# Optimization experiments

Hardware: AMD Instinct MI355X
Metric: run time of the kernel (lower is better)

Reference implementation:

```python
import jax, jax.numpy as jnp
import numpy as np

WORD_DICT_SIZE = 50002
POS_DICT_SIZE = 53
DEP_DICT_SIZE = 54
EMB = 128
UNITS = 100
B, T = 256, 256
IN_DIM = 3 * EMB  # 384


def setup_inputs() -> dict:
    key = jax.random.key(0)
    ks = jax.random.split(key, 12)
    words = jax.random.randint(ks[0], (B, T), 1, WORD_DICT_SIZE)
    pos = jax.random.randint(ks[1], (B, T), 1, POS_DICT_SIZE)
    dep = jax.random.randint(ks[2], (B, T), 1, DEP_DICT_SIZE)
    # ragged padding: index 0 is the mask token (mask_zero=True)
    lengths = jax.random.randint(ks[3], (B,), T // 2, T + 1)
    pad = jnp.arange(T)[None, :] >= lengths[:, None]
    words = jnp.where(pad, 0, words)
    pos = jnp.where(pad, 0, pos)
    dep = jnp.where(pad, 0, dep)

    def glorot(k, shape):
        lim = np.sqrt(6.0 / (shape[0] + shape[1]))
        return jax.random.uniform(k, shape, jnp.float32, -lim, lim)

    E_word = glorot(ks[4], (WORD_DICT_SIZE, EMB))
    E_pos = glorot(ks[5], (POS_DICT_SIZE, EMB))
    E_dep = glorot(ks[6], (DEP_DICT_SIZE, EMB))
    W_fwd = glorot(ks[7], (IN_DIM, 4 * UNITS))
    U_fwd = glorot(ks[8], (UNITS, 4 * UNITS))
    W_bwd = glorot(ks[9], (IN_DIM, 4 * UNITS))
    U_bwd = glorot(ks[10], (UNITS, 4 * UNITS))
    # Keras unit_forget_bias=True: forget-gate bias initialized to 1
    b = jnp.zeros((4 * UNITS,), jnp.float32).at[UNITS:2 * UNITS].set(1.0)
    W_out = glorot(ks[11], (2 * UNITS, 1))
    b_out = jnp.zeros((1,), jnp.float32)
    return {"words": words, "pos": pos, "dep": dep,
            "E_word": E_word, "E_pos": E_pos, "E_dep": E_dep,
            "W_fwd": W_fwd, "U_fwd": U_fwd, "b_fwd": b,
            "W_bwd": W_bwd, "U_bwd": U_bwd, "b_bwd": b,
            "W_out": W_out, "b_out": b_out}


def _masked_lstm(x_tbd, mask_tb, W, U, b, reverse):
    """Keras-style masked LSTM. x_tbd: [T,B,D], mask_tb: [T,B].
    Masked steps carry state/output through unchanged (zero_output_for_mask=False)."""
    units = U.shape[0]
    xw = jnp.einsum('tbd,dh->tbh', x_tbd, W) + b  # precompute input projection

    def step(carry, inp):
        h, c = carry
        xw_t, m = inp
        z = xw_t + h @ U
        i, f, g, o = jnp.split(z, 4, axis=-1)
        i = jax.nn.sigmoid(i)
        f = jax.nn.sigmoid(f)
        g = jnp.tanh(g)
        o = jax.nn.sigmoid(o)
        c_new = f * c + i * g
        h_new = o * jnp.tanh(c_new)
        m = m[:, None]
        h2 = jnp.where(m, h_new, h)
        c2 = jnp.where(m, c_new, c)
        return (h2, c2), h2

    h0 = jnp.zeros((x_tbd.shape[1], units), x_tbd.dtype)
    _, hs = jax.lax.scan(step, (h0, h0), (xw, mask_tb), reverse=reverse)
    return hs  # [T,B,units]


def reference(words, pos, dep, E_word, E_pos, E_dep,
              W_fwd, U_fwd, b_fwd, W_bwd, U_bwd, b_bwd, W_out, b_out):
    mask = words != 0  # [B,T]
    x = jnp.concatenate([E_word[words], E_pos[pos], E_dep[dep]], axis=-1)  # [B,T,384]
    xt = jnp.transpose(x, (1, 0, 2))  # [T,B,384]
    mt = mask.T                        # [T,B]
    h_f = _masked_lstm(xt, mt, W_fwd, U_fwd, b_fwd, reverse=False)
    h_b = _masked_lstm(xt, mt, W_bwd, U_bwd, b_bwd, reverse=True)
    h = jnp.concatenate([h_f, h_b], axis=-1)          # [T,B,200]
    h = jnp.transpose(h, (1, 0, 2))                    # [B,T,200]
    out = jax.nn.sigmoid(h @ W_out + b_out)[..., 0]    # [B,T]
    return out
```

## Files before the change

### kernel.cpp

```cpp
#include <hip/hip_runtime.h>
#include <hip/hip_bf16.h>

#define T_LEN 256
#define B_SZ  256
#define EMB   128
#define UNITS 100
#define GATES 400
#define NCOL  800
#define NQ    52

typedef __attribute__((ext_vector_type(8))) short short8v;
typedef __attribute__((ext_vector_type(4))) short short4v;
typedef __attribute__((ext_vector_type(4))) float f32x4;
typedef _Float16 half2v __attribute__((ext_vector_type(2)));

static __device__ __forceinline__ float bf2f(short s) {
    unsigned u = ((unsigned)(unsigned short)s) << 16;
    return __builtin_bit_cast(float, u);
}
static __device__ __forceinline__ short f2bf(float f) {
    return __builtin_bit_cast(short, __float2bfloat16(f));
}
static __device__ __forceinline__ float fast_sigmoid(float x) {
    return 1.f / (1.f + __expf(-x));
}
static __device__ __forceinline__ float fast_tanh(float x) {
    return 1.f - 2.f / (1.f + __expf(2.f * x));
}
static __device__ __forceinline__ float fdot2p(unsigned hp, unsigned up, float c) {
#if __has_builtin(__builtin_amdgcn_fdot2)
    return __builtin_amdgcn_fdot2(__builtin_bit_cast(half2v, hp),
                                  __builtin_bit_cast(half2v, up), c, false);
#else
    const half2v a = __builtin_bit_cast(half2v, hp);
    const half2v b = __builtin_bit_cast(half2v, up);
    return fmaf((float)a[1], (float)b[1], fmaf((float)a[0], (float)b[0], c));
#endif
}

#define PREP_WT_BLOCKS 100
#define PREP_TAB_BLOCKS 107
#define PREP_UPK_BLOCKS 21

__global__ __launch_bounds__(256) void prep(
    const float* __restrict__ Wf, const float* __restrict__ Wb,
    const float* __restrict__ bf_, const float* __restrict__ bb_,
    const float* __restrict__ Ep, const float* __restrict__ Ed,
    const float* __restrict__ Uf, const float* __restrict__ Ub,
    __hip_bfloat16* __restrict__ WbT, float* __restrict__ Ppos,
    float* __restrict__ Pdep, unsigned* __restrict__ Upk, int* __restrict__ flag)
{
    __shared__ short Ap[16 * 32];
    __shared__ short Bp[32 * 16];

    const int bx = blockIdx.x, tid = threadIdx.x;

    if (bx < PREP_WT_BLOCKS) {
        const int base = bx * 1024 + tid * 4;
#pragma unroll
        for (int q = 0; q < 4; ++q) {
            const int id = base + q;
            const int c = id >> 7, k = id & 127;
            const int dir = c >= GATES;
            const int j = c - dir * GATES;
            const float* W = dir ? Wb : Wf;
            WbT[id] = __float2bfloat16(W[k * GATES + j]);
        }
    } else if (bx < PREP_WT_BLOCKS + PREP_TAB_BLOCKS) {
        const int p = bx - PREP_WT_BLOCKS;
        const bool isPos = p < 53;
        const float* Erow = isPos ? (Ep + p * EMB) : (Ed + (size_t)(p - 53) * EMB);
        const int rowoff = isPos ? EMB : 2 * EMB;
        float* dst = isPos ? (Ppos + (size_t)p * NCOL) : (Pdep + (size_t)(p - 53) * NCOL);
        for (int c = tid; c < NCOL; c += 256) {
            const int dir = c >= GATES;
            const int j = c - dir * GATES;
            const float* W = dir ? Wb : Wf;
            float s = 0.f;
            for (int k = 0; k < EMB; ++k)
                s = fmaf(Erow[k], W[(size_t)(rowoff + k) * GATES + j], s);
            if (!isPos) s += (dir ? bb_[j] : bf_[j]);
            dst[c] = s;
        }
    } else if (bx < PREP_WT_BLOCKS + PREP_TAB_BLOCKS + PREP_UPK_BLOCKS) {
        const int p2 = bx - PREP_WT_BLOCKS - PREP_TAB_BLOCKS;
#pragma unroll
        for (int i = 0; i < 8; ++i) {
            const int e = p2 * 2048 + tid * 8 + i;
            if (e < 2 * NQ * GATES) {
                const int dir = e / (NQ * GATES);
                const int rem = e - dir * (NQ * GATES);
                const int q = rem / GATES, col = rem - q * GATES;
                const float* U = dir ? Ub : Uf;
                const int k0 = 2 * q, k1 = 2 * q + 1;
                const float v0 = (k0 < UNITS) ? U[(size_t)k0 * GATES + col] : 0.f;
                const float v1 = (k1 < UNITS) ? U[(size_t)k1 * GATES + col] : 0.f;
                const unsigned lo = (unsigned)(unsigned short)__builtin_bit_cast(short, (_Float16)v0);
                const unsigned hi = (unsigned)(unsigned short)__builtin_bit_cast(short, (_Float16)v1);
                Upk[e] = lo | (hi << 16);
            }
        }
    } else {
        if (tid < 64) {
            for (int e = tid; e < 512; e += 64) {
                const int m = e >> 5, k = e & 31;
                Ap[e] = f2bf((float)((m * 3 + k * 5) % 7 - 3));
            }
            for (int e = tid; e < 512; e += 64) {
                const int k = e >> 4, n = e & 15;
                Bp[e] = f2bf((float)((k * 7 + n * 3) % 5 - 2));
            }
        }
        __syncthreads();
        if (tid < 64) {
            const int l = tid, mn = l & 15, grp = l >> 4;
            float ref[4];
#pragma unroll
            for (int i = 0; i < 4; ++i) {
                const int m = grp * 4 + i;
                float s = 0.f;
                for (int k = 0; k < 32; ++k)
                    s += bf2f(Ap[m * 32 + k]) * bf2f(Bp[k * 16 + mn]);
                ref[i] = s;
            }
            short8v a8, b8;
#pragma unroll
            for (int e = 0; e < 8; ++e) {
                const int k8 = grp * 8 + e;
                a8[e] = Ap[mn * 32 + k8];
                b8[e] = Bp[k8 * 16 + mn];
            }
            f32x4 z = {0.f, 0.f, 0.f, 0.f};
            f32x4 d8 = __builtin_amdgcn_mfma_f32_16x16x32_bf16(a8, b8, z, 0, 0, 0);
            const bool ok8 = (d8[0] == ref[0]) && (d8[1] == ref[1]) &&
                             (d8[2] == ref[2]) && (d8[3] == ref[3]);
            const unsigned long long m8 = __ballot(ok8);
            if (tid == 0) flag[0] = (m8 == ~0ULL) ? 0 : 1;
        }
    }
}

#define MT 64
#define NT 160

__global__ __launch_bounds__(256) void embed_gemm(
    const int* __restrict__ words, const int* __restrict__ pos, const int* __restrict__ dep,
    const float* __restrict__ Ew, const __hip_bfloat16* __restrict__ WbT,
    const float* __restrict__ Ppos, const float* __restrict__ Pdep,
    const int* __restrict__ flag, __hip_bfloat16* __restrict__ xw)
{
    __shared__ __align__(16) short As[MT * 128];
    __shared__ __align__(16) short Bs[NT * 128];
    __shared__ int widx[MT], pidx[MT], didx[MT];

    const int tid = threadIdx.x;
    const int bx = blockIdx.x, by = blockIdx.y;
    const int r0 = bx * MT;
    const int t = r0 >> 8, b0 = r0 & 255;
    const int n0 = by * NT;

    if (tid < MT)             widx[tid]          = words[(size_t)(b0 + tid) * T_LEN + t];
    else if (tid < 2 * MT)    pidx[tid - MT]     = pos[(size_t)(b0 + tid - MT) * T_LEN + t];
    else if (tid < 3 * MT)    didx[tid - 2 * MT] = dep[(size_t)(b0 + tid - 2 * MT) * T_LEN + t];
    __syncthreads();

#pragma unroll
    for (int q = 0; q < 4; ++q) {
        const int ch = tid + q * 256;
        const int row = ch >> 4, c16 = ch & 15;
        const float* src = Ew + (size_t)widx[row] * EMB + c16 * 8;
        const float4 v0 = *reinterpret_cast<const float4*>(src);
        const float4 v1 = *reinterpret_cast<const float4*>(src + 4);
        short8v pk;
        pk[0] = f2bf(v0.x); pk[1] = f2bf(v0.y); pk[2] = f2bf(v0.z); pk[3] = f2bf(v0.w);
        pk[4] = f2bf(v1.x); pk[5] = f2bf(v1.y); pk[6] = f2bf(v1.z); pk[7] = f2bf(v1.w);
        *reinterpret_cast<short8v*>(&As[row * 128 + ((c16 ^ (row & 7)) << 3)]) = pk;
    }
#pragma unroll
    for (int q = 0; q < 10; ++q) {
        const int ch = tid + q * 256;
        const int col = ch >> 4, c16 = ch & 15;
        const short* src = reinterpret_cast<const short*>(WbT) + (size_t)(n0 + col) * 128 + c16 * 8;
        const short8v v = *reinterpret_cast<const short8v*>(src);
        *reinterpret_cast<short8v*>(&Bs[col * 128 + ((c16 ^ (col & 7)) << 3)]) = v;
    }
    __syncthreads();

    const int w = tid >> 6, l = tid & 63;
    const int lr = l & 15, lg = l >> 4;
    const int arow = w * 16 + lr;

    f32x4 acc[10];
#pragma unroll
    for (int ni = 0; ni < 10; ++ni) acc[ni] = f32x4{0.f, 0.f, 0.f, 0.f};

    const int lay = flag[0];

    if (lay == 0) {
#pragma unroll
        for (int kk = 0; kk < 4; ++kk) {
            const int c16 = kk * 4 + lg;
            const short8v a = *reinterpret_cast<const short8v*>(
                &As[arow * 128 + ((c16 ^ (arow & 7)) << 3)]);
#pragma unroll
            for (int ni = 0; ni < 10; ++ni) {
                const int col = ni * 16 + lr;
                const short8v bfr = *reinterpret_cast<const short8v*>(
                    &Bs[col * 128 + ((c16 ^ (col & 7)) << 3)]);
                acc[ni] = __builtin_amdgcn_mfma_f32_16x16x32_bf16(a, bfr, acc[ni], 0, 0, 0);
            }
        }
    } else {
#pragma unroll
        for (int kk = 0; kk < 4; ++kk) {
            const int ch16 = kk * 4 + (lg >> 1);
            const int inner = (lg & 1) * 4;
            const int alo_i = arow * 128 + ((ch16 ^ (arow & 7)) << 3) + inner;
            const int ahi_i = arow * 128 + (((ch16 + 2) ^ (arow & 7)) << 3) + inner;
            const short4v alo = *reinterpret_cast<const short4v*>(&As[alo_i]);
            const short4v ahi = *reinterpret_cast<const short4v*>(&As[ahi_i]);
            short8v a;
            a[0] = alo[0]; a[1] = alo[1]; a[2] = alo[2]; a[3] = alo[3];
            a[4] = ahi[0]; a[5] = ahi[1]; a[6] = ahi[2]; a[7] = ahi[3];
#pragma unroll
            for (int ni = 0; ni < 10; ++ni) {
                const int col = ni * 16 + lr;
                const int blo_i = col * 128 + ((ch16 ^ (col & 7)) << 3) + inner;
                const int bhi_i = col * 128 + (((ch16 + 2) ^ (col & 7)) << 3) + inner;
                const short4v blo = *reinterpret_cast<const short4v*>(&Bs[blo_i]);
                const short4v bhi = *reinterpret_cast<const short4v*>(&Bs[bhi_i]);
                short8v b;
                b[0] = blo[0]; b[1] = blo[1]; b[2] = blo[2]; b[3] = blo[3];
                b[4] = bhi[0]; b[5] = bhi[1]; b[6] = bhi[2]; b[7] = bhi[3];
                acc[ni] = __builtin_amdgcn_mfma_f32_16x16x32_bf16(a, b, acc[ni], 0, 0, 0);
            }
        }
    }

    const int rbase = w * 16 + lg * 4;
    int pix[4], dix[4];
#pragma unroll
    for (int i = 0; i < 4; ++i) { pix[i] = pidx[rbase + i]; dix[i] = didx[rbase + i]; }
#pragma unroll
    for (int ni = 0; ni < 10; ++ni) {
        const int c = n0 + ni * 16 + lr;
#pragma unroll
        for (int i = 0; i < 4; ++i) {
            const float v = acc[ni][i]
                          + Ppos[(size_t)pix[i] * NCOL + c]
                          + Pdep[(size_t)dix[i] * NCOL + c];
            xw[(size_t)(r0 + rbase + i) * NCOL + c] = __float2bfloat16(v);
        }
    }
}

#define BAR() do { \
    asm volatile("s_waitcnt lgkmcnt(0)" ::: "memory"); \
    __builtin_amdgcn_sched_barrier(0); \
    __builtin_amdgcn_s_barrier(); \
    __builtin_amdgcn_sched_barrier(0); \
} while (0)

__global__ __launch_bounds__(512, 1) void lstm_valu(
    const int* __restrict__ words,
    const __hip_bfloat16* __restrict__ xw,
    const unsigned* __restrict__ Upk,
    _Float16* __restrict__ h_f, _Float16* __restrict__ h_b)
{
    const int b = blockIdx.x >> 1, dirv = blockIdx.x & 1;
    _Float16* hout = dirv ? h_b : h_f;
    const int coff = dirv * GATES;
    const unsigned* up = Upk + (size_t)dirv * NQ * GATES;

    __shared__ __align__(16) _Float16 h_sh[104];
    __shared__ float z_sh[GATES];
    __shared__ unsigned char m_sh[T_LEN];
    __shared__ int len_sh;

    const int tid = threadIdx.x;
    const bool isCol = tid < GATES;
    const int colid = isCol ? tid : (GATES - 1);

    for (int i = tid; i < T_LEN; i += 512)
        m_sh[i] = (unsigned char)(words[(size_t)b * T_LEN + i] != 0);
    if (tid < 52) reinterpret_cast<unsigned*>(h_sh)[tid] = 0u;

    unsigned upk[NQ];
#pragma unroll
    for (int q = 0; q < NQ; ++q) upk[q] = up[q * GATES + colid];
#pragma unroll
    for (int q = 0; q < NQ; ++q) asm volatile("" : "+v"(upk[q]));

    float c = 0.f, h = 0.f;
    __syncthreads();

    if (tid == 0) {
        int fmi = T_LEN;
        for (int t = 0; t < T_LEN; ++t) if (!m_sh[t]) { fmi = t; break; }
        int ok = 1;
        for (int t = fmi; t < T_LEN; ++t) if (m_sh[t]) { ok = 0; break; }
        len_sh = ok ? fmi : T_LEN;
    }
    __syncthreads();
    const int len = len_sh;

    const short* xs = reinterpret_cast<const short*>(xw);

    if (dirv && tid < UNITS) {
        for (int t = len; t < T_LEN; ++t)
            hout[((size_t)t * B_SZ + b) * UNITS + tid] = (_Float16)0.f;
    }

    short pf = 0;
    if (isCol && len > 0) {
        const int tfirst = dirv ? (len - 1) : 0;
        pf = xs[((size_t)tfirst * B_SZ + b) * NCOL + coff + tid];
    }

    for (int s = 0; s < len; ++s) {
        const int t = dirv ? (len - 1 - s) : s;
        int tn = dirv ? (t - 1) : (t + 1);
        tn = tn < 0 ? 0 : (tn > T_LEN - 1 ? T_LEN - 1 : tn);

        short pfn = pf;
        if (isCol) {
            const float zx = bf2f(pf);
            pfn = xs[((size_t)tn * B_SZ + b) * NCOL + coff + tid];
            float a0 = 0.f, a1 = 0.f, a2 = 0.f, a3 = 0.f;
            const uint4* h4 = reinterpret_cast<const uint4*>(h_sh);
#pragma unroll
            for (int qq = 0; qq < 13; ++qq) {
                const uint4 hv = h4[qq];
                a0 = fdot2p(hv.x, upk[4 * qq + 0], a0);
                a1 = fdot2p(hv.y, upk[4 * qq + 1], a1);
                a2 = fdot2p(hv.z, upk[4 * qq + 2], a2);
                a3 = fdot2p(hv.w, upk[4 * qq + 3], a3);
            }
            z_sh[tid] = zx + (a0 + a1) + (a2 + a3);
        }
        pf = pfn;

        BAR();

        if (tid < UNITS) {
            const float zi = z_sh[tid];
            const float zf = z_sh[tid + UNITS];
            const float zg = z_sh[tid + 2 * UNITS];
            const float zo = z_sh[tid + 3 * UNITS];
            const float ig = fast_sigmoid(zi);
            const float fg = fast_sigmoid(zf);
            const float gg = fast_tanh(zg);
            const float og = fast_sigmoid(zo);
            const float cn = fg * c + ig * gg;
            const float hn = og * fast_tanh(cn);
            const bool  m  = m_sh[t] != 0;
            h = m ? hn : h;
            c = m ? cn : c;
            const _Float16 hh = (_Float16)h;
            h_sh[tid] = hh;
            hout[((size_t)t * B_SZ + b) * UNITS + tid] = hh;
        }

        BAR();
    }

    if (!dirv && tid < UNITS) {
        const _Float16 hh = (_Float16)h;
        for (int t = len; t < T_LEN; ++t)
            hout[((size_t)t * B_SZ + b) * UNITS + tid] = hh;
    }
}

__global__ __launch_bounds__(256) void out_proj(
    const _Float16* __restrict__ h_f, const _Float16* __restrict__ h_b,
    const float* __restrict__ Wo, const float* __restrict__ bo,
    float* __restrict__ out)
{
    const int tid = threadIdx.x;
    const int g = tid >> 2, sub = tid & 3;
    const int r = blockIdx.x * 64 + g;
    const int t = r >> 8, b = r & 255;

    const _Float16* hf = h_f + (size_t)r * UNITS;
    const _Float16* hb = h_b + (size_t)r * UNITS;

    float s = 0.f;
    const int k0 = sub * 25;
#pragma unroll
    for (int k = 0; k < 25; ++k) s = fmaf((float)hf[k0 + k], Wo[k0 + k], s);
#pragma unroll
    for (int k = 0; k < 25; ++k) s = fmaf((float)hb[k0 + k], Wo[UNITS + k0 + k], s);

    s += __shfl_xor(s, 1);
    s += __shfl_xor(s, 2);

    if (sub == 0)
        out[(size_t)b * T_LEN + t] = 1.f / (1.f + __expf(-(s + bo[0])));
}

extern "C" void kernel_launch(void* const* d_in, const int* in_sizes, int n_in,
                              void* d_out, int out_size, void* d_ws, size_t ws_size,
                              hipStream_t stream)
{
    const int*   words = (const int*)d_in[0];
    const int*   pos   = (const int*)d_in[1];
    const int*   dep   = (const int*)d_in[2];
    const float* Ew    = (const float*)d_in[3];
    const float* Ep    = (const float*)d_in[4];
    const float* Ed    = (const float*)d_in[5];
    const float* Wf    = (const float*)d_in[6];
    const float* Uf    = (const float*)d_in[7];
    const float* bf_   = (const float*)d_in[8];
    const float* Wb    = (const float*)d_in[9];
    const float* Ub    = (const float*)d_in[10];
    const float* bb_   = (const float*)d_in[11];
    const float* Wo    = (const float*)d_in[12];
    const float* bo    = (const float*)d_in[13];
    float* out = (float*)d_out;

    auto alignup = [](size_t x) { return (x + 255) & ~(size_t)255; };
    char* p = (char*)d_ws;
    __hip_bfloat16* xw = (__hip_bfloat16*)p;  p += alignup((size_t)T_LEN * B_SZ * NCOL * 2);
    _Float16* h_f = (_Float16*)p;             p += alignup((size_t)T_LEN * B_SZ * UNITS * 2);
    _Float16* h_b = (_Float16*)p;             p += alignup((size_t)T_LEN * B_SZ * UNITS * 2);
    __hip_bfloat16* WbT = (__hip_bfloat16*)p; p += alignup((size_t)NCOL * 128 * 2);
    float* Ppos = (float*)p;                  p += alignup((size_t)53 * NCOL * 4);
    float* Pdep = (float*)p;                  p += alignup((size_t)54 * NCOL * 4);
    unsigned* Upk = (unsigned*)p;             p += alignup((size_t)2 * NQ * GATES * 4);
    int* flag = (int*)p;

    prep<<<dim3(PREP_WT_BLOCKS + PREP_TAB_BLOCKS + PREP_UPK_BLOCKS + 1), 256, 0, stream>>>(
        Wf, Wb, bf_, bb_, Ep, Ed, Uf, Ub, WbT, Ppos, Pdep, Upk, flag);

    embed_gemm<<<dim3((T_LEN * B_SZ) / MT, NCOL / NT), 256, 0, stream>>>(
        words, pos, dep, Ew, WbT, Ppos, Pdep, flag, xw);

    lstm_valu<<<dim3(B_SZ * 2), 512, 0, stream>>>(words, xw, Upk, h_f, h_b);

    out_proj<<<dim3((T_LEN * B_SZ) / 64), 256, 0, stream>>>(h_f, h_b, Wo, bo, out);
}
```

Baseline: 347.7 us.

## Run each LSTM direction recurrence in a single wavefront without block barriers

Replaces the 512-thread-per-sequence recurrence with a single 64-lane wavefront, where each lane owns 7 gate columns (350 packed U registers) and two hidden units. The U matrix is repacked so the four gates of a unit sit next to each other, which lets each lane read its gates with float4 LDS loads and lets all cross-thread exchange rely on wave-level LDS waits rather than s_barrier. This removes two workgroup barriers per timestep. In exchange each lane does about 7x more dot-product work per step, and the very large register footprint risks spills and leaves only one wave per block on the GPU.

```diff
diff --git a/kernel.cpp b/kernel.cpp
--- a/kernel.cpp
+++ b/kernel.cpp
@@ -7,7 +7,9 @@
 #define UNITS 100
 #define GATES 400
 #define NCOL  800
-#define NQ    52
+#define NPP   50
+#define CPL   7
+#define JPAD  448
 
 typedef __attribute__((ext_vector_type(8))) short short8v;
 typedef __attribute__((ext_vector_type(4))) short short4v;
@@ -40,7 +42,7 @@
 
 #define PREP_WT_BLOCKS 100
 #define PREP_TAB_BLOCKS 107
-#define PREP_UPK_BLOCKS 21
+#define PREP_UPK_BLOCKS 22
 
 __global__ __launch_bounds__(256) void prep(
     const float* __restrict__ Wf, const float* __restrict__ Wb,
@@ -87,17 +89,22 @@
 #pragma unroll
         for (int i = 0; i < 8; ++i) {
             const int e = p2 * 2048 + tid * 8 + i;
-            if (e < 2 * NQ * GATES) {
-                const int dir = e / (NQ * GATES);
-                const int rem = e - dir * (NQ * GATES);
-                const int q = rem / GATES, col = rem - q * GATES;
-                const float* U = dir ? Ub : Uf;
-                const int k0 = 2 * q, k1 = 2 * q + 1;
-                const float v0 = (k0 < UNITS) ? U[(size_t)k0 * GATES + col] : 0.f;
-                const float v1 = (k1 < UNITS) ? U[(size_t)k1 * GATES + col] : 0.f;
-                const unsigned lo = (unsigned)(unsigned short)__builtin_bit_cast(short, (_Float16)v0);
-                const unsigned hi = (unsigned)(unsigned short)__builtin_bit_cast(short, (_Float16)v1);
-                Upk[e] = lo | (hi << 16);
+            if (e < 2 * NPP * JPAD) {
+                const int dir = e / (NPP * JPAD);
+                const int rem = e - dir * (NPP * JPAD);
+                const int p = rem / JPAD, jp = rem - p * JPAD;
+                unsigned val = 0u;
+                if (jp < GATES) {
+                    const int unit = jp >> 2, gate = jp & 3;
+                    const int jorig = gate * UNITS + unit;
+                    const float* U = dir ? Ub : Uf;
+                    const float v0 = U[(size_t)(2 * p) * GATES + jorig];
+                    const float v1 = U[(size_t)(2 * p + 1) * GATES + jorig];
+                    const unsigned lo = (unsigned)(unsigned short)__builtin_bit_cast(short, (_Float16)v0);
+                    const unsigned hi = (unsigned)(unsigned short)__builtin_bit_cast(short, (_Float16)v1);
+                    val = lo | (hi << 16);
+                }
+                Upk[e] = val;
             }
         }
     } else {
@@ -254,14 +261,7 @@
     }
 }
 
-#define BAR() do { \
-    asm volatile("s_waitcnt lgkmcnt(0)" ::: "memory"); \
-    __builtin_amdgcn_sched_barrier(0); \
-    __builtin_amdgcn_s_barrier(); \
-    __builtin_amdgcn_sched_barrier(0); \
-} while (0)
-
-__global__ __launch_bounds__(512, 1) void lstm_valu(
+__global__ __launch_bounds__(64, 1) void lstm_wave(
     const int* __restrict__ words,
     const __hip_bfloat16* __restrict__ xw,
     const unsigned* __restrict__ Upk,
@@ -269,52 +269,75 @@
 {
     const int b = blockIdx.x >> 1, dirv = blockIdx.x & 1;
     _Float16* hout = dirv ? h_b : h_f;
+    const unsigned* up = Upk + (size_t)dirv * (NPP * JPAD);
     const int coff = dirv * GATES;
-    const unsigned* up = Upk + (size_t)dirv * NQ * GATES;
-
-    __shared__ __align__(16) _Float16 h_sh[104];
-    __shared__ float z_sh[GATES];
+
+    __shared__ __align__(16) float zs[JPAD];
+    __shared__ __align__(16) unsigned hp_sh[52];
     __shared__ unsigned char m_sh[T_LEN];
     __shared__ int len_sh;
 
-    const int tid = threadIdx.x;
-    const bool isCol = tid < GATES;
-    const int colid = isCol ? tid : (GATES - 1);
-
-    for (int i = tid; i < T_LEN; i += 512)
-        m_sh[i] = (unsigned char)(words[(size_t)b * T_LEN + i] != 0);
-    if (tid < 52) reinterpret_cast<unsigned*>(h_sh)[tid] = 0u;
-
-    unsigned upk[NQ];
-#pragma unroll
-    for (int q = 0; q < NQ; ++q) upk[q] = up[q * GATES + colid];
-#pragma unroll
-    for (int q = 0; q < NQ; ++q) asm volatile("" : "+v"(upk[q]));
-
-    float c = 0.f, h = 0.f;
-    __syncthreads();
-
-    if (tid == 0) {
+    const int lane = threadIdx.x;
+
+#pragma unroll
+    for (int i = 0; i < 4; ++i)
+        m_sh[lane + 64 * i] =
+            (unsigned char)(words[(size_t)b * T_LEN + lane + 64 * i] != 0);
+    if (lane < 52) hp_sh[lane] = 0u;
+
+    unsigned upk[CPL][NPP];
+#pragma unroll
+    for (int c = 0; c < CPL; ++c)
+#pragma unroll
+        for (int p = 0; p < NPP; ++p)
+            upk[c][p] = up[p * JPAD + lane * CPL + c];
+#pragma unroll
+    for (int c = 0; c < CPL; ++c)
+#pragma unroll
+        for (int p = 0; p < NPP; ++p)
+            asm volatile("" : "+v"(upk[c][p]));
+
+    int xoff[CPL];
+#pragma unroll
+    for (int c = 0; c < CPL; ++c) {
+        const int jp = lane * CPL + c;
+        if (jp < GATES) {
+            const int unit = jp >> 2, gate = jp & 3;
+            xoff[c] = coff + gate * UNITS + unit;
+        } else {
+            xoff[c] = coff;
+        }
+    }
+
+    float c0 = 0.f, c1 = 0.f, h0 = 0.f, h1 = 0.f;
+
+    asm volatile("s_waitcnt lgkmcnt(0)" ::: "memory");
+
+    if (lane == 0) {
         int fmi = T_LEN;
         for (int t = 0; t < T_LEN; ++t) if (!m_sh[t]) { fmi = t; break; }
         int ok = 1;
         for (int t = fmi; t < T_LEN; ++t) if (m_sh[t]) { ok = 0; break; }
         len_sh = ok ? fmi : T_LEN;
     }
-    __syncthreads();
+    asm volatile("s_waitcnt lgkmcnt(0)" ::: "memory");
     const int len = len_sh;
 
+    if (dirv && lane < NPP) {
+        for (int t = len; t < T_LEN; ++t)
+            *reinterpret_cast<unsigned*>(
+                &hout[((size_t)t * B_SZ + b) * UNITS + 2 * lane]) = 0u;
+    }
+
     const short* xs = reinterpret_cast<const short*>(xw);
-
-    if (dirv && tid < UNITS) {
-        for (int t = len; t < T_LEN; ++t)
-            hout[((size_t)t * B_SZ + b) * UNITS + tid] = (_Float16)0.f;
-    }
-
-    short pf = 0;
-    if (isCol && len > 0) {
+    short pf[CPL];
+#pragma unroll
+    for (int c = 0; c < CPL; ++c) pf[c] = 0;
+    if (len > 0) {
         const int tfirst = dirv ? (len - 1) : 0;
-        pf = xs[((size_t)tfirst * B_SZ + b) * NCOL + coff + tid];
+#pragma unroll
+        for (int c = 0; c < CPL; ++c)
+            pf[c] = xs[((size_t)tfirst * B_SZ + b) * NCOL + xoff[c]];
     }
 
     for (int s = 0; s < len; ++s) {
@@ -322,52 +345,69 @@
         int tn = dirv ? (t - 1) : (t + 1);
         tn = tn < 0 ? 0 : (tn > T_LEN - 1 ? T_LEN - 1 : tn);
 
-        short pfn = pf;
-        if (isCol) {
-            const float zx = bf2f(pf);
-            pfn = xs[((size_t)tn * B_SZ + b) * NCOL + coff + tid];
-            float a0 = 0.f, a1 = 0.f, a2 = 0.f, a3 = 0.f;
-            const uint4* h4 = reinterpret_cast<const uint4*>(h_sh);
-#pragma unroll
-            for (int qq = 0; qq < 13; ++qq) {
-                const uint4 hv = h4[qq];
-                a0 = fdot2p(hv.x, upk[4 * qq + 0], a0);
-                a1 = fdot2p(hv.y, upk[4 * qq + 1], a1);
-                a2 = fdot2p(hv.z, upk[4 * qq + 2], a2);
-                a3 = fdot2p(hv.w, upk[4 * qq + 3], a3);
-            }
-            z_sh[tid] = zx + (a0 + a1) + (a2 + a3);
-        }
-        pf = pfn;
-
-        BAR();
-
-        if (tid < UNITS) {
-            const float zi = z_sh[tid];
-            const float zf = z_sh[tid + UNITS];
-            const float zg = z_sh[tid + 2 * UNITS];
-            const float zo = z_sh[tid + 3 * UNITS];
-            const float ig = fast_sigmoid(zi);
-            const float fg = fast_sigmoid(zf);
-            const float gg = fast_tanh(zg);
-            const float og = fast_sigmoid(zo);
-            const float cn = fg * c + ig * gg;
-            const float hn = og * fast_tanh(cn);
-            const bool  m  = m_sh[t] != 0;
-            h = m ? hn : h;
-            c = m ? cn : c;
-            const _Float16 hh = (_Float16)h;
-            h_sh[tid] = hh;
-            hout[((size_t)t * B_SZ + b) * UNITS + tid] = hh;
-        }
-
-        BAR();
-    }
-
-    if (!dirv && tid < UNITS) {
-        const _Float16 hh = (_Float16)h;
+        float acc[CPL];
+#pragma unroll
+        for (int c = 0; c < CPL; ++c) acc[c] = bf2f(pf[c]);
+#pragma unroll
+        for (int c = 0; c < CPL; ++c)
+            pf[c] = xs[((size_t)tn * B_SZ + b) * NCOL + xoff[c]];
+
+#pragma unroll
+        for (int pp = 0; pp < 13; ++pp) {
+            const uint4 hv = *reinterpret_cast<const uint4*>(&hp_sh[4 * pp]);
+            const unsigned he[4] = {hv.x, hv.y, hv.z, hv.w};
+#pragma unroll
+            for (int e = 0; e < 4; ++e) {
+                const int p = 4 * pp + e;
+                if (p < NPP) {
+#pragma unroll
+                    for (int c = 0; c < CPL; ++c)
+                        acc[c] = fdot2p(he[e], upk[c][p], acc[c]);
+                }
+            }
+        }
+
+#pragma unroll
+        for (int c = 0; c < CPL; ++c) zs[lane * CPL + c] = acc[c];
+        asm volatile("s_waitcnt lgkmcnt(0)" ::: "memory");
+        __builtin_amdgcn_sched_barrier(0);
+
+        if (lane < NPP) {
+            const float4 z0 = *reinterpret_cast<const float4*>(&zs[8 * lane]);
+            const float4 z1 = *reinterpret_cast<const float4*>(&zs[8 * lane + 4]);
+            const bool m = m_sh[t] != 0;
+            {
+                const float ig = fast_sigmoid(z0.x), fg = fast_sigmoid(z0.y);
+                const float gg = fast_tanh(z0.z),    og = fast_sigmoid(z0.w);
+                const float cn = fg * c0 + ig * gg;
+                const float hn = og * fast_tanh(cn);
+                h0 = m ? hn : h0;  c0 = m ? cn : c0;
+            }
+            {
+                const float ig = fast_sigmoid(z1.x), fg = fast_sigmoid(z1.y);
+                const float gg = fast_tanh(z1.z),    og = fast_sigmoid(z1.w);
+                const float cn = fg * c1 + ig * gg;
+                const float hn = og * fast_tanh(cn);
+                h1 = m ? hn : h1;  c1 = m ? cn : c1;
+            }
+            const unsigned hpk =
+                (unsigned)(unsigned short)__builtin_bit_cast(short, (_Float16)h0) |
+                ((unsigned)(unsigned short)__builtin_bit_cast(short, (_Float16)h1) << 16);
+            hp_sh[lane] = hpk;
+            *reinterpret_cast<unsigned*>(
+                &hout[((size_t)t * B_SZ + b) * UNITS + 2 * lane]) = hpk;
+        }
+        asm volatile("s_waitcnt lgkmcnt(0)" ::: "memory");
+        __builtin_amdgcn_sched_barrier(0);
+    }
+
+    if (!dirv && lane < NPP) {
+        const unsigned hpk =
+            (unsigned)(unsigned short)__builtin_bit_cast(short, (_Float16)h0) |
+            ((unsigned)(unsigned short)__builtin_bit_cast(short, (_Float16)h1) << 16);
         for (int t = len; t < T_LEN; ++t)
-            hout[((size_t)t * B_SZ + b) * UNITS + tid] = hh;
+            *reinterpret_cast<unsigned*>(
+                &hout[((size_t)t * B_SZ + b) * UNITS + 2 * lane]) = hpk;
     }
 }
 
@@ -426,7 +466,7 @@
     __hip_bfloat16* WbT = (__hip_bfloat16*)p; p += alignup((size_t)NCOL * 128 * 2);
     float* Ppos = (float*)p;                  p += alignup((size_t)53 * NCOL * 4);
     float* Pdep = (float*)p;                  p += alignup((size_t)54 * NCOL * 4);
-    unsigned* Upk = (unsigned*)p;             p += alignup((size_t)2 * NQ * GATES * 4);
+    unsigned* Upk = (unsigned*)p;             p += alignup((size_t)2 * NPP * JPAD * 4);
     int* flag = (int*)p;
 
     prep<<<dim3(PREP_WT_BLOCKS + PREP_TAB_BLOCKS + PREP_UPK_BLOCKS + 1), 256, 0, stream>>>(
@@ -435,7 +475,7 @@
     embed_gemm<<<dim3((T_LEN * B_SZ) / MT, NCOL / NT), 256, 0, stream>>>(
         words, pos, dep, Ew, WbT, Ppos, Pdep, flag, xw);
 
-    lstm_valu<<<dim3(B_SZ * 2), 512, 0, stream>>>(words, xw, Upk, h_f, h_b);
+    lstm_wave<<<dim3(B_SZ * 2), 64, 0, stream>>>(words, xw, Upk, h_f, h_b);
 
     out_proj<<<dim3((T_LEN * B_SZ) / 64), 256, 0, stream>>>(h_f, h_b, Wo, bo, out);
 }
```

After: 530.1 us. +52.5%, slower.

## Compute all four gates per unit thread with double-buffered hidden state

Applied to the files above, without the earlier changes.

The LSTM recurrence kernel goes from 512 threads (one per gate column, with a z_sh exchange and two barriers per step) to 128 threads where each unit thread holds all four gate columns of U in registers. The packed recurrent weights are reordered so each thread's gate columns are contiguous. The hidden state is double-buffered in shared memory, so each step needs one barrier instead of two and no cross-thread gate exchange. The cost is 208 weight registers per thread and four times more dot-product work per thread on fewer waves, which may lengthen the serial per-step latency.

```diff
diff --git a/kernel.cpp b/kernel.cpp
--- a/kernel.cpp
+++ b/kernel.cpp
@@ -90,11 +90,13 @@
             if (e < 2 * NQ * GATES) {
                 const int dir = e / (NQ * GATES);
                 const int rem = e - dir * (NQ * GATES);
-                const int q = rem / GATES, col = rem - q * GATES;
+                const int q = rem / GATES, jp = rem - q * GATES;
+                const int unit = jp >> 2, gate = jp & 3;
+                const int jorig = gate * UNITS + unit;
                 const float* U = dir ? Ub : Uf;
                 const int k0 = 2 * q, k1 = 2 * q + 1;
-                const float v0 = (k0 < UNITS) ? U[(size_t)k0 * GATES + col] : 0.f;
-                const float v1 = (k1 < UNITS) ? U[(size_t)k1 * GATES + col] : 0.f;
+                const float v0 = (k0 < UNITS) ? U[(size_t)k0 * GATES + jorig] : 0.f;
+                const float v1 = (k1 < UNITS) ? U[(size_t)k1 * GATES + jorig] : 0.f;
                 const unsigned lo = (unsigned)(unsigned short)__builtin_bit_cast(short, (_Float16)v0);
                 const unsigned hi = (unsigned)(unsigned short)__builtin_bit_cast(short, (_Float16)v1);
                 Upk[e] = lo | (hi << 16);
@@ -261,7 +263,7 @@
     __builtin_amdgcn_sched_barrier(0); \
 } while (0)
 
-__global__ __launch_bounds__(512, 1) void lstm_valu(
+__global__ __launch_bounds__(128, 1) void lstm_unit(
     const int* __restrict__ words,
     const __hip_bfloat16* __restrict__ xw,
     const unsigned* __restrict__ Upk,
@@ -272,24 +274,29 @@
     const int coff = dirv * GATES;
     const unsigned* up = Upk + (size_t)dirv * NQ * GATES;
 
-    __shared__ __align__(16) _Float16 h_sh[104];
-    __shared__ float z_sh[GATES];
+    __shared__ __align__(16) _Float16 h_buf[2][104];
     __shared__ unsigned char m_sh[T_LEN];
     __shared__ int len_sh;
 
     const int tid = threadIdx.x;
-    const bool isCol = tid < GATES;
-    const int colid = isCol ? tid : (GATES - 1);
-
-    for (int i = tid; i < T_LEN; i += 512)
-        m_sh[i] = (unsigned char)(words[(size_t)b * T_LEN + i] != 0);
-    if (tid < 52) reinterpret_cast<unsigned*>(h_sh)[tid] = 0u;
-
-    unsigned upk[NQ];
-#pragma unroll
-    for (int q = 0; q < NQ; ++q) upk[q] = up[q * GATES + colid];
-#pragma unroll
-    for (int q = 0; q < NQ; ++q) asm volatile("" : "+v"(upk[q]));
+    const bool isUnit = tid < UNITS;
+    const int ul = isUnit ? tid : (UNITS - 1);
+
+    m_sh[tid]       = (unsigned char)(words[(size_t)b * T_LEN + tid] != 0);
+    m_sh[tid + 128] = (unsigned char)(words[(size_t)b * T_LEN + tid + 128] != 0);
+    if (tid < 104) reinterpret_cast<unsigned*>(&h_buf[0][0])[tid] = 0u;
+
+    unsigned upk[4][NQ];
+#pragma unroll
+    for (int g = 0; g < 4; ++g)
+#pragma unroll
+        for (int q = 0; q < NQ; ++q)
+            upk[g][q] = up[q * GATES + 4 * ul + g];
+#pragma unroll
+    for (int g = 0; g < 4; ++g)
+#pragma unroll
+        for (int q = 0; q < NQ; ++q)
+            asm volatile("" : "+v"(upk[g][q]));
 
     float c = 0.f, h = 0.f;
     __syncthreads();
@@ -304,70 +311,80 @@
     __syncthreads();
     const int len = len_sh;
 
+    if (dirv && isUnit) {
+        for (int t = len; t < T_LEN; ++t)
+            hout[((size_t)t * B_SZ + b) * UNITS + ul] = (_Float16)0.f;
+    }
+
     const short* xs = reinterpret_cast<const short*>(xw);
-
-    if (dirv && tid < UNITS) {
-        for (int t = len; t < T_LEN; ++t)
-            hout[((size_t)t * B_SZ + b) * UNITS + tid] = (_Float16)0.f;
-    }
-
-    short pf = 0;
-    if (isCol && len > 0) {
+    short pf[4];
+#pragma unroll
+    for (int g = 0; g < 4; ++g) pf[g] = 0;
+    if (len > 0) {
         const int tfirst = dirv ? (len - 1) : 0;
-        pf = xs[((size_t)tfirst * B_SZ + b) * NCOL + coff + tid];
-    }
-
+#pragma unroll
+        for (int g = 0; g < 4; ++g)
+            pf[g] = xs[((size_t)tfirst * B_SZ + b) * NCOL + coff + g * UNITS + ul];
+    }
+
+    int p = 0;
     for (int s = 0; s < len; ++s) {
         const int t = dirv ? (len - 1 - s) : s;
         int tn = dirv ? (t - 1) : (t + 1);
         tn = tn < 0 ? 0 : (tn > T_LEN - 1 ? T_LEN - 1 : tn);
 
-        short pfn = pf;
-        if (isCol) {
-            const float zx = bf2f(pf);
-            pfn = xs[((size_t)tn * B_SZ + b) * NCOL + coff + tid];
-            float a0 = 0.f, a1 = 0.f, a2 = 0.f, a3 = 0.f;
-            const uint4* h4 = reinterpret_cast<const uint4*>(h_sh);
-#pragma unroll
-            for (int qq = 0; qq < 13; ++qq) {
-                const uint4 hv = h4[qq];
-                a0 = fdot2p(hv.x, upk[4 * qq + 0], a0);
-                a1 = fdot2p(hv.y, upk[4 * qq + 1], a1);
-                a2 = fdot2p(hv.z, upk[4 * qq + 2], a2);
-                a3 = fdot2p(hv.w, upk[4 * qq + 3], a3);
-            }
-            z_sh[tid] = zx + (a0 + a1) + (a2 + a3);
-        }
-        pf = pfn;
-
-        BAR();
-
-        if (tid < UNITS) {
-            const float zi = z_sh[tid];
-            const float zf = z_sh[tid + UNITS];
-            const float zg = z_sh[tid + 2 * UNITS];
-            const float zo = z_sh[tid + 3 * UNITS];
-            const float ig = fast_sigmoid(zi);
-            const float fg = fast_sigmoid(zf);
-            const float gg = fast_tanh(zg);
-            const float og = fast_sigmoid(zo);
+        float acc[4];
+#pragma unroll
+        for (int g = 0; g < 4; ++g) acc[g] = bf2f(pf[g]);
+#pragma unroll
+        for (int g = 0; g < 4; ++g)
+            pf[g] = xs[((size_t)tn * B_SZ + b) * NCOL + coff + g * UNITS + ul];
+
+        const uint4* h4 = reinterpret_cast<const uint4*>(&h_buf[p][0]);
+#pragma unroll
+        for (int pp = 0; pp < 13; ++pp) {
+            const uint4 hv = h4[pp];
+            acc[0] = fdot2p(hv.x, upk[0][4 * pp + 0], acc[0]);
+            acc[1] = fdot2p(hv.x, upk[1][4 * pp + 0], acc[1]);
+            acc[2] = fdot2p(hv.x, upk[2][4 * pp + 0], acc[2]);
+            acc[3] = fdot2p(hv.x, upk[3][4 * pp + 0], acc[3]);
+            acc[0] = fdot2p(hv.y, upk[0][4 * pp + 1], acc[0]);
+            acc[1] = fdot2p(hv.y, upk[1][4 * pp + 1], acc[1]);
+            acc[2] = fdot2p(hv.y, upk[2][4 * pp + 1], acc[2]);
+            acc[3] = fdot2p(hv.y, upk[3][4 * pp + 1], acc[3]);
+            acc[0] = fdot2p(hv.z, upk[0][4 * pp + 2], acc[0]);
+            acc[1] = fdot2p(hv.z, upk[1][4 * pp + 2], acc[1]);
+            acc[2] = fdot2p(hv.z, upk[2][4 * pp + 2], acc[2]);
+            acc[3] = fdot2p(hv.z, upk[3][4 * pp + 2], acc[3]);
+            acc[0] = fdot2p(hv.w, upk[0][4 * pp + 3], acc[0]);
+            acc[1] = fdot2p(hv.w, upk[1][4 * pp + 3], acc[1]);
+            acc[2] = fdot2p(hv.w, upk[2][4 * pp + 3], acc[2]);
+            acc[3] = fdot2p(hv.w, upk[3][4 * pp + 3], acc[3]);
+        }
+
+        if (isUnit) {
+            const float ig = fast_sigmoid(acc[0]);
+            const float fg = fast_sigmoid(acc[1]);
+            const float gg = fast_tanh(acc[2]);
+            const float og = fast_sigmoid(acc[3]);
             const float cn = fg * c + ig * gg;
             const float hn = og * fast_tanh(cn);
-            const bool  m  = m_sh[t] != 0;
+            const bool m = m_sh[t] != 0;
             h = m ? hn : h;
             c = m ? cn : c;
             const _Float16 hh = (_Float16)h;
-            h_sh[tid] = hh;
-            hout[((size_t)t * B_SZ + b) * UNITS + tid] = hh;
+            h_buf[p ^ 1][ul] = hh;
+            hout[((size_t)t * B_SZ + b) * UNITS + ul] = hh;
         }
 
         BAR();
-    }
-
-    if (!dirv && tid < UNITS) {
+        p ^= 1;
+    }
+
+    if (!dirv && isUnit) {
         const _Float16 hh = (_Float16)h;
         for (int t = len; t < T_LEN; ++t)
-            hout[((size_t)t * B_SZ + b) * UNITS + tid] = hh;
+            hout[((size_t)t * B_SZ + b) * UNITS + ul] = hh;
     }
 }
 
@@ -435,7 +452,7 @@
     embed_gemm<<<dim3((T_LEN * B_SZ) / MT, NCOL / NT), 256, 0, stream>>>(
         words, pos, dep, Ew, WbT, Ppos, Pdep, flag, xw);
 
-    lstm_valu<<<dim3(B_SZ * 2), 512, 0, stream>>>(words, xw, Upk, h_f, h_b);
+    lstm_unit<<<dim3(B_SZ * 2), 128, 0, stream>>>(words, xw, Upk, h_f, h_b);
 
     out_proj<<<dim3((T_LEN * B_SZ) / 64), 256, 0, stream>>>(h_f, h_b, Wo, bo, out);
 }
```

After: 421.6 us. 21.3% more time.
